# Kernel tuning notes

Hardware: AMD Instinct MI355X
Metric: run time of the kernel (lower is better)

The kernel has to match this reference:

```python
import jax, jax.numpy as jnp
import numpy as np

PHI = (1.0 + 5.0 ** 0.5) / 2.0
B, S, V, D, N, L = 8, 128, 32000, 256, 256, 2


def silu(x):
    return x * jax.nn.sigmoid(x)


def setup_inputs() -> dict:
    key = jax.random.key(0)
    ks = jax.random.split(key, 9)
    inp = {}
    inp["input_ids"] = jax.random.randint(ks[0], (B, S), 0, V)
    # token embedding, init std=0.02 as in _init_weights
    inp["emb"] = 0.02 * jax.random.normal(ks[1], (V, 2 * D), jnp.float32)
    # per-layer resonant params, stacked over layer dim L
    inp["ip_w"] = 0.02 * jax.random.normal(ks[2], (L, D, 2 * D), jnp.float32)  # input_proj weight
    inp["ip_b"] = jnp.zeros((L, D), jnp.float32)                                # input_proj bias
    inp["Wn"] = 0.02 * jax.random.normal(ks[3], (L, N, D), jnp.float32)         # W parameter
    inp["Bn"] = jnp.zeros((L, N, D), jnp.float32)                               # B parameter
    inp["opr"] = 0.02 * jax.random.normal(ks[4], (L, D, N), jnp.float32)        # out_proj_real
    inp["opi"] = 0.02 * jax.random.normal(ks[5], (L, D, N), jnp.float32)        # out_proj_imag
    inp["out_w"] = 0.02 * jax.random.normal(ks[6], (V, 2 * D), jnp.float32)     # output_proj
    inp["out_b"] = jnp.zeros((V,), jnp.float32)
    return inp


def _forward(input_ids, emb, ip_w, ip_b, Wn, Bn, opr, opi, out_w, out_b):
    tok = emb[input_ids]                                  # [B, S, 2D]
    w_emb = jnp.transpose(tok[..., :D], (1, 0, 2))        # [S, B, D] (time-major for scan)
    b_emb = jnp.transpose(tok[..., D:], (1, 0, 2))        # [S, B, D]
    ts = jnp.arange(S, dtype=jnp.float32)                 # t values

    def step(carry, xs):
        h_r, h_i = carry
        w_t, b_t, t = xs
        t_phi = t * PHI
        # Euler transform of recurrent state
        wl = 1.0 + jnp.abs(w_t)                           # [B, D]
        th_r = h_r / wl + b_t + t_phi
        th_i = h_i / wl + b_t + t_phi
        sr, cr = jnp.sin(th_r), jnp.cos(th_r)
        si, ci = jnp.sin(th_i), jnp.cos(th_i)
        h_r_new = cr * ci - sr * si                       # complex rotate
        h_i_new = cr * si + sr * ci
        x_r, x_i = h_r_new, h_i_new
        # resonant layers (residual deltas)
        for l in range(L):
            xc = jnp.concatenate([x_r, x_i], axis=-1) @ ip_w[l].T + ip_b[l]   # [B, D]
            wl_n = 1.0 + jnp.abs(Wn[l])                                        # [N, D]
            theta = xc[:, None, :] / wl_n + Bn[l] + t_phi                      # [B, N, D]
            cos_sum = jnp.cos(theta).sum(-1)                                   # [B, N]
            sin_sum = jnp.sin(theta).sum(-1)                                   # [B, N]
            x_r = x_r + silu(cos_sum @ opr[l].T)
            x_i = x_i + silu(sin_sum @ opi[l].T)
        logits = jnp.concatenate([x_r, x_i], axis=-1) @ out_w.T + out_b       # [B, V]
        return (h_r_new, h_i_new), logits

    h0 = jnp.zeros((B, D), jnp.float32)
    (_, _), logits = jax.lax.scan(step, (h0, h0), (w_emb, b_emb, ts))
    return jnp.transpose(logits, (1, 0, 2))               # [B, S, V]


def reference(input_ids, emb, ip_w, ip_b, Wn, Bn, opr, opi, out_w, out_b):
    return _forward(input_ids, emb, ip_w, ip_b, Wn, Bn, opr, opi, out_w, out_b)
```

## Files before the change

### kernel.cpp

```cpp
#include <hip/hip_runtime.h>
#include <hip/hip_fp16.h>
#include <math.h>


#define PHIF 1.6180339887498949f

typedef unsigned short u16;
typedef __attribute__((ext_vector_type(8))) _Float16 f16x8;
typedef __attribute__((ext_vector_type(4))) float f32x4;

constexpr int B = 8, S = 128, V = 32000, D = 256, N = 256, L = 2;
constexpr int TWO_D = 512;
constexpr int M = S * B;

constexpr size_t OFF_XR   = 0;
constexpr size_t OFF_XI   = OFF_XR   + (size_t)M * D;
constexpr size_t OFF_XC   = OFF_XI   + (size_t)M * D;
constexpr size_t OFF_CS   = OFF_XC   + (size_t)M * D;
constexpr size_t OFF_SS   = OFF_CS   + (size_t)M * N;
constexpr size_t OFF_RWT  = OFF_SS   + (size_t)M * N;
constexpr size_t OFF_BNT  = OFF_RWT  + (size_t)L * N * D;
constexpr size_t OFF_IPWT = OFF_BNT  + (size_t)L * N * D;
constexpr size_t OFF_OPRT = OFF_IPWT + (size_t)L * TWO_D * D;
constexpr size_t OFF_OPIT = OFF_OPRT + (size_t)L * N * D;
constexpr size_t OFF_FLT_END = OFF_OPIT + (size_t)L * N * D;

constexpr size_t A2_BYTE_OFF = OFF_FLT_END * 4;
constexpr size_t W2_BYTE_OFF = A2_BYTE_OFF + (size_t)M * 512 * 2;
constexpr size_t WS_NEED     = W2_BYTE_OFF + (size_t)V * 512 * 2;

__device__ __forceinline__ u16 f2h(float x) {
    return __half_as_ushort(__float2half(x));
}

__global__ void prep_kernel(const float* __restrict__ Wn,
                            const float* __restrict__ Bn,
                            const float* __restrict__ ip_w,
                            const float* __restrict__ opr,
                            const float* __restrict__ opi,
                            float* __restrict__ ws) {
    int i = blockIdx.x * blockDim.x + threadIdx.x;
    if (i < L * N * D) {
        int l = i >> 16;
        int r = i & 65535;
        int a = r >> 8;
        int c = r & 255;
        float wv = Wn[(size_t)l * N * D + (size_t)c * D + a];
        ws[OFF_RWT + i] = 1.0f / (1.0f + fabsf(wv));
        ws[OFF_BNT + i] = Bn[(size_t)l * N * D + (size_t)c * D + a];
        ws[OFF_OPRT + i] = opr[(size_t)l * D * N + (size_t)c * N + a];
        ws[OFF_OPIT + i] = opi[(size_t)l * D * N + (size_t)c * N + a];
    }
    if (i < L * TWO_D * D) {
        int l = i >> 17;
        int r = i & 131071;
        int k = r >> 8;
        int d = r & 255;
        ws[OFF_IPWT + i] = ip_w[(size_t)l * D * TWO_D + (size_t)d * TWO_D + k];
    }
}

__global__ __launch_bounds__(256) void conv_w_kernel(const float* __restrict__ out_w,
                                                     u16* __restrict__ W2) {
    int gid = blockIdx.x * blockDim.x + threadIdx.x;
    if (gid >= V * 128) return;
    int v  = gid >> 7;
    int kq = (gid & 127) << 2;
    float4 x = *(const float4*)&out_w[(size_t)v * TWO_D + kq];
    ushort4 h = {f2h(x.x), f2h(x.y), f2h(x.z), f2h(x.w)};
    *(ushort4*)&W2[(size_t)v * 512 + kq] = h;
}

__global__ __launch_bounds__(256) void conv_a_kernel(const float* __restrict__ ws,
                                                     u16* __restrict__ A2) {
    int gid = blockIdx.x * blockDim.x + threadIdx.x;
    if (gid >= M * 128) return;
    int m  = gid >> 7;
    int kq = (gid & 127) << 2;
    const float* XR = ws + OFF_XR;
    const float* XI = ws + OFF_XI;
    float4 x = (kq < D) ? *(const float4*)&XR[(size_t)m * D + kq]
                        : *(const float4*)&XI[(size_t)m * D + kq - D];
    ushort4 h = {f2h(x.x), f2h(x.y), f2h(x.z), f2h(x.w)};
    *(ushort4*)&A2[(size_t)m * 512 + kq] = h;
}

__global__ void recur_kernel(const int* __restrict__ ids,
                             const float* __restrict__ emb,
                             float* __restrict__ ws) {
    int tid = blockIdx.x * blockDim.x + threadIdx.x;
    if (tid >= B * D) return;
    int b = tid >> 8;
    int d = tid & 255;
    float* XR = ws + OFF_XR;
    float* XI = ws + OFF_XI;
    float hr = 0.f, hi = 0.f;
    for (int t = 0; t < S; ++t) {
        int id = ids[b * S + t];
        const float* e = emb + (size_t)id * TWO_D;
        float w  = e[d];
        float bb = e[D + d];
        float wl = 1.0f + fabsf(w);
        float tphi = (float)t * PHIF;
        float thr = hr / wl + bb + tphi;
        float thi = hi / wl + bb + tphi;
        float sr, cr, si, ci;
        sincosf(thr, &sr, &cr);
        sincosf(thi, &si, &ci);
        float nhr = cr * ci - sr * si;
        float nhi = cr * si + sr * ci;
        int row = t * B + b;
        XR[row * D + d] = nhr;
        XI[row * D + d] = nhi;
        hr = nhr; hi = nhi;
    }
}

__global__ __launch_bounds__(256) void xc_kernel(const float* __restrict__ ipb,
                                                 int l,
                                                 float* __restrict__ ws) {
    __shared__ float xrow[8][TWO_D];
    const float* XR = ws + OFF_XR;
    const float* XI = ws + OFF_XI;
    const float* WT = ws + OFF_IPWT + (size_t)l * TWO_D * D;
    float* XC = ws + OFF_XC;
    int m0 = blockIdx.x * 8;
    int tid = threadIdx.x;
    for (int j = 0; j < 16; ++j) {
        int idx = tid + j * 256;
        int r = idx >> 9;
        int k = idx & 511;
        xrow[r][k] = (k < D) ? XR[(m0 + r) * D + k] : XI[(m0 + r) * D + (k - D)];
    }
    __syncthreads();
    int d = tid;
    float bias = ipb[l * D + d];
    float acc[8];
    #pragma unroll
    for (int r = 0; r < 8; ++r) acc[r] = bias;
    for (int k = 0; k < TWO_D; ++k) {
        float wv = WT[k * D + d];
        #pragma unroll
        for (int r = 0; r < 8; ++r) acc[r] = fmaf(xrow[r][k], wv, acc[r]);
    }
    #pragma unroll
    for (int r = 0; r < 8; ++r) XC[(m0 + r) * D + d] = acc[r];
}

__global__ __launch_bounds__(256) void theta_kernel(int l, float* __restrict__ ws) {
    __shared__ float xls[2][D];
    const float* RWT = ws + OFF_RWT + (size_t)l * D * N;
    const float* BNT = ws + OFF_BNT + (size_t)l * D * N;
    const float* XC = ws + OFF_XC;
    float* CS = ws + OFF_CS;
    float* SS = ws + OFF_SS;
    int tb0 = blockIdx.x * 2;
    int n = threadIdx.x;
    xls[0][n] = XC[(size_t)tb0 * D + n];
    xls[1][n] = XC[(size_t)(tb0 + 1) * D + n];
    __syncthreads();
    float tp0 = (float)(tb0 >> 3) * PHIF;
    float tp1 = (float)((tb0 + 1) >> 3) * PHIF;
    float ac0 = 0.f, as0 = 0.f, ac1 = 0.f, as1 = 0.f;
    #pragma unroll 4
    for (int d = 0; d < D; ++d) {
        float rw = RWT[d * N + n];
        float bn = BNT[d * N + n];
        float th0 = fmaf(xls[0][d], rw, bn) + tp0;
        float th1 = fmaf(xls[1][d], rw, bn) + tp1;
        ac0 += __cosf(th0); as0 += __sinf(th0);
        ac1 += __cosf(th1); as1 += __sinf(th1);
    }
    CS[(size_t)tb0 * N + n] = ac0;
    SS[(size_t)tb0 * N + n] = as0;
    CS[(size_t)(tb0 + 1) * N + n] = ac1;
    SS[(size_t)(tb0 + 1) * N + n] = as1;
}

__global__ __launch_bounds__(256) void update_kernel(int l, float* __restrict__ ws) {
    __shared__ float csh[8][N];
    __shared__ float ssh[8][N];
    const float* CS = ws + OFF_CS;
    const float* SS = ws + OFF_SS;
    const float* WR = ws + OFF_OPRT + (size_t)l * N * D;
    const float* WI = ws + OFF_OPIT + (size_t)l * N * D;
    float* XR = ws + OFF_XR;
    float* XI = ws + OFF_XI;
    int m0 = blockIdx.x * 8;
    int tid = threadIdx.x;
    for (int j = 0; j < 8; ++j) {
        int idx = tid + j * 256;
        int r = idx >> 8;
        int n = idx & 255;
        csh[r][n] = CS[(m0 + r) * N + n];
        ssh[r][n] = SS[(m0 + r) * N + n];
    }
    __syncthreads();
    int d = tid;
    float accr[8] = {0,0,0,0,0,0,0,0};
    float acci[8] = {0,0,0,0,0,0,0,0};
    for (int n = 0; n < N; ++n) {
        float wr = WR[n * D + d];
        float wi = WI[n * D + d];
        #pragma unroll
        for (int r = 0; r < 8; ++r) {
            accr[r] = fmaf(csh[r][n], wr, accr[r]);
            acci[r] = fmaf(ssh[r][n], wi, acci[r]);
        }
    }
    #pragma unroll
    for (int r = 0; r < 8; ++r) {
        float vr = accr[r], vi = acci[r];
        float sgr = 1.0f / (1.0f + expf(-vr));
        float sgi = 1.0f / (1.0f + expf(-vi));
        XR[(m0 + r) * D + d] += vr * sgr;
        XI[(m0 + r) * D + d] += vi * sgi;
    }
}

__global__ __launch_bounds__(256) void logits_mfma_kernel(const u16* __restrict__ A2,
                                                          const u16* __restrict__ W2,
                                                          const float* __restrict__ out_b,
                                                          float* __restrict__ out) {
    __shared__ u16 sA[128 * 32];
    __shared__ u16 sW[128 * 32];
    int cb = blockIdx.x % (V / 128);
    int rb = blockIdx.x / (V / 128);
    int tid = threadIdx.x;
    int w = tid >> 6, l = tid & 63;
    int wr = w >> 1, wc = w & 1;

    f32x4 acc[4][4];
    #pragma unroll
    for (int i = 0; i < 4; ++i)
        #pragma unroll
        for (int j = 0; j < 4; ++j) acc[i][j] = (f32x4){0.f, 0.f, 0.f, 0.f};

    int srow = l >> 2;
    int sko  = (l & 3) * 8;
    int kg = (l >> 4) * 8;
    int rl = l & 15;

    for (int kk = 0; kk < 512; kk += 32) {
        #pragma unroll
        for (int j = 0; j < 2; ++j) {
            int rloc = (w * 2 + j) * 16 + srow;
            const u16* sa = A2 + (size_t)(rb * 128 + rloc) * 512 + kk + sko;
            const u16* sw = W2 + (size_t)(cb * 128 + rloc) * 512 + kk + sko;
            u16* da = &sA[rloc * 32 + sko];
            u16* dw = &sW[rloc * 32 + sko];
            __builtin_amdgcn_global_load_lds((const __attribute__((address_space(1))) void*)sa,
                                             (__attribute__((address_space(3))) void*)da, 16, 0, 0);
            __builtin_amdgcn_global_load_lds((const __attribute__((address_space(1))) void*)sw,
                                             (__attribute__((address_space(3))) void*)dw, 16, 0, 0);
        }
        __syncthreads();
        f16x8 af[4], wf[4];
        #pragma unroll
        for (int f = 0; f < 4; ++f) {
            af[f] = *(const f16x8*)&sA[(wr * 64 + f * 16 + rl) * 32 + kg];
            wf[f] = *(const f16x8*)&sW[(wc * 64 + f * 16 + rl) * 32 + kg];
        }
        #pragma unroll
        for (int fr = 0; fr < 4; ++fr)
            #pragma unroll
            for (int fc = 0; fc < 4; ++fc)
                acc[fr][fc] = __builtin_amdgcn_mfma_f32_16x16x32_f16(
                    af[fr], wf[fc], acc[fr][fc], 0, 0, 0);
        __syncthreads();
    }

    int rq = l >> 4;
    #pragma unroll
    for (int fc = 0; fc < 4; ++fc) {
        int v = cb * 128 + wc * 64 + fc * 16 + rl;
        float bv = out_b[v];
        #pragma unroll
        for (int fr = 0; fr < 4; ++fr) {
            #pragma unroll
            for (int r = 0; r < 4; ++r) {
                int row = rb * 128 + wr * 64 + fr * 16 + rq * 4 + r;
                int t = row >> 3, b = row & 7;
                out[((size_t)(b * S + t)) * V + v] = acc[fr][fc][r] + bv;
            }
        }
    }
}

constexpr int GBM = 256, GBN = 64, GBK = 32;
constexpr int LDA = GBM + 4;
constexpr int LDW = GBN + 4;

__global__ __launch_bounds__(256) void logits_kernel(const float* __restrict__ out_w,
                                                     const float* __restrict__ out_b,
                                                     const float* __restrict__ ws,
                                                     float* __restrict__ out) {
    __shared__ float As[GBK][LDA];
    __shared__ float Wsh[GBK][LDW];
    const float* XR = ws + OFF_XR;
    const float* XI = ws + OFF_XI;
    int cb = blockIdx.x % (V / GBN);
    int rb = blockIdx.x / (V / GBN);
    int tid = threadIdx.x;
    int tx = tid & 7;
    int ty = tid >> 3;
    int m_base = ty * 8;
    int n0 = tx * 8;
    float acc[8][8];
    #pragma unroll
    for (int r = 0; r < 8; ++r)
        #pragma unroll
        for (int c = 0; c < 8; ++c) acc[r][c] = 0.f;

    for (int kc = 0; kc < TWO_D; kc += GBK) {
        #pragma unroll
        for (int j = 0; j < 32; ++j) {
            int idx = tid + j * 256;
            int k = idx & 31;
            int m = idx >> 5;
            int kgl = kc + k;
            int row = rb * GBM + m;
            As[k][m] = (kgl < D) ? XR[row * D + kgl] : XI[row * D + (kgl - D)];
        }
        #pragma unroll
        for (int j = 0; j < 8; ++j) {
            int idx = tid + j * 256;
            int k = idx & 31;
            int n = idx >> 5;
            Wsh[k][n] = out_w[(size_t)(cb * GBN + n) * TWO_D + kc + k];
        }
        __syncthreads();
        #pragma unroll 8
        for (int k = 0; k < GBK; ++k) {
            float4 a0 = *(const float4*)&As[k][m_base];
            float4 a1 = *(const float4*)&As[k][m_base + 4];
            float4 w0 = *(const float4*)&Wsh[k][n0];
            float4 w1 = *(const float4*)&Wsh[k][n0 + 4];
            float am[8] = {a0.x, a0.y, a0.z, a0.w, a1.x, a1.y, a1.z, a1.w};
            float wn[8] = {w0.x, w0.y, w0.z, w0.w, w1.x, w1.y, w1.z, w1.w};
            #pragma unroll
            for (int r = 0; r < 8; ++r)
                #pragma unroll
                for (int c = 0; c < 8; ++c)
                    acc[r][c] = fmaf(am[r], wn[c], acc[r][c]);
        }
        __syncthreads();
    }
    int v0 = cb * GBN + n0;
    float4 ob0 = *(const float4*)&out_b[v0];
    float4 ob1 = *(const float4*)&out_b[v0 + 4];
    float obn[8] = {ob0.x, ob0.y, ob0.z, ob0.w, ob1.x, ob1.y, ob1.z, ob1.w};
    #pragma unroll
    for (int r = 0; r < 8; ++r) {
        int row = rb * GBM + m_base + r;
        int t = row >> 3;
        int b = row & 7;
        float o[8];
        #pragma unroll
        for (int c = 0; c < 8; ++c) o[c] = acc[r][c] + obn[c];
        *(float4*)&out[((size_t)(b * S + t)) * V + v0]     = *(float4*)&o[0];
        *(float4*)&out[((size_t)(b * S + t)) * V + v0 + 4] = *(float4*)&o[4];
    }
}

extern "C" void kernel_launch(void* const* d_in, const int* in_sizes, int n_in,
                              void* d_out, int out_size, void* d_ws, size_t ws_size,
                              hipStream_t stream) {
    const int*   ids   = (const int*)d_in[0];
    const float* emb   = (const float*)d_in[1];
    const float* ip_w  = (const float*)d_in[2];
    const float* ip_b  = (const float*)d_in[3];
    const float* Wn    = (const float*)d_in[4];
    const float* Bn    = (const float*)d_in[5];
    const float* opr   = (const float*)d_in[6];
    const float* opi   = (const float*)d_in[7];
    const float* out_w = (const float*)d_in[8];
    const float* out_b = (const float*)d_in[9];
    float* out = (float*)d_out;
    float* ws  = (float*)d_ws;
    const bool use_mfma = (ws_size >= WS_NEED);
    u16* A2 = (u16*)((char*)d_ws + A2_BYTE_OFF);
    u16* W2 = (u16*)((char*)d_ws + W2_BYTE_OFF);

    hipLaunchKernelGGL(prep_kernel,  dim3(1024), dim3(256), 0, stream, Wn, Bn, ip_w, opr, opi, ws);
    if (use_mfma)
        hipLaunchKernelGGL(conv_w_kernel, dim3(V * 128 / 256), dim3(256), 0, stream, out_w, W2);
    hipLaunchKernelGGL(recur_kernel, dim3(32),   dim3(64),  0, stream, ids, emb, ws);
    for (int l = 0; l < L; ++l) {
        hipLaunchKernelGGL(xc_kernel,     dim3(M / 8), dim3(256), 0, stream, ip_b, l, ws);
        hipLaunchKernelGGL(theta_kernel,  dim3(M / 2), dim3(256), 0, stream, l, ws);
        hipLaunchKernelGGL(update_kernel, dim3(M / 8), dim3(256), 0, stream, l, ws);
    }
    if (use_mfma) {
        hipLaunchKernelGGL(conv_a_kernel, dim3(M * 128 / 256), dim3(256), 0, stream, ws, A2);
        hipLaunchKernelGGL(logits_mfma_kernel, dim3((V / 128) * (M / 128)), dim3(256), 0, stream,
                           A2, W2, out_b, out);
    } else {
        hipLaunchKernelGGL(logits_kernel, dim3((V / GBN) * (M / GBM)), dim3(256), 0, stream,
                           out_w, out_b, ws, out);
    }
}
```

Baseline: 585.1 us.

## Collapse complex rotation into one phase and prefetch embeddings in recurrence

The recurrence is rewritten using the identity that the two rotations compose into a single angle, psi = (hr+hi)/wl + 2b + 2t*phi. Each step then needs one sin/cos pair, evaluated with the fast __sinf/__cosf intrinsics, instead of two full sincosf calls. Embedding rows for the whole sequence are prefetched into shared memory, which takes the dependent global loads off the serial critical path. Separately, the logits GEMM block order is swapped so consecutive blocks share a weight column tile, which should improve L2 reuse. The trade-off is that fast intrinsics on arguments reaching a few hundred radians may lose accuracy.

New measurement: 495.0 us. -15.4%, faster.

```diff
diff --git a/kernel.cpp b/kernel.cpp
--- a/kernel.cpp
+++ b/kernel.cpp
@@ -85,34 +85,40 @@
     *(ushort4*)&A2[(size_t)m * 512 + kq] = h;
 }
 
-__global__ void recur_kernel(const int* __restrict__ ids,
-                             const float* __restrict__ emb,
-                             float* __restrict__ ws) {
-    int tid = blockIdx.x * blockDim.x + threadIdx.x;
-    if (tid >= B * D) return;
-    int b = tid >> 8;
-    int d = tid & 255;
+__global__ __launch_bounds__(64) void recur_kernel(const int* __restrict__ ids,
+                                                   const float* __restrict__ emb,
+                                                   float* __restrict__ ws) {
+    __shared__ int   sid[S];
+    __shared__ float swv[S][64];
+    __shared__ float sbv[S][64];
+    int lane = threadIdx.x;
+    int blk  = blockIdx.x;
+    int b  = blk >> 2;
+    int d  = (blk & 3) * 64 + lane;
+    sid[lane]      = ids[b * S + lane];
+    sid[64 + lane] = ids[b * S + 64 + lane];
+    __syncthreads();
+    #pragma unroll 16
+    for (int t = 0; t < S; ++t) {
+        const float* e = emb + (size_t)sid[t] * TWO_D;
+        swv[t][lane] = e[d];
+        sbv[t][lane] = e[D + d];
+    }
+    __syncthreads();
     float* XR = ws + OFF_XR;
     float* XI = ws + OFF_XI;
-    float hr = 0.f, hi = 0.f;
+    float u = 0.f;
+    #pragma unroll 8
     for (int t = 0; t < S; ++t) {
-        int id = ids[b * S + t];
-        const float* e = emb + (size_t)id * TWO_D;
-        float w  = e[d];
-        float bb = e[D + d];
-        float wl = 1.0f + fabsf(w);
-        float tphi = (float)t * PHIF;
-        float thr = hr / wl + bb + tphi;
-        float thi = hi / wl + bb + tphi;
-        float sr, cr, si, ci;
-        sincosf(thr, &sr, &cr);
-        sincosf(thi, &si, &ci);
-        float nhr = cr * ci - sr * si;
-        float nhi = cr * si + sr * ci;
-        int row = t * B + b;
-        XR[row * D + d] = nhr;
-        XI[row * D + d] = nhi;
-        hr = nhr; hi = nhi;
+        float wl = 1.0f + fabsf(swv[t][lane]);
+        float c  = 2.0f * sbv[t][lane] + (2.0f * PHIF) * (float)t;
+        float psi = __fdividef(u, wl) + c;
+        float sn = __sinf(psi);
+        float cs = __cosf(psi);
+        size_t row = (size_t)(t * B + b) * D + d;
+        XR[row] = cs;
+        XI[row] = sn;
+        u = cs + sn;
     }
 }
 
@@ -224,8 +230,8 @@
                                                           float* __restrict__ out) {
     __shared__ u16 sA[128 * 32];
     __shared__ u16 sW[128 * 32];
-    int cb = blockIdx.x % (V / 128);
-    int rb = blockIdx.x / (V / 128);
+    int rb = blockIdx.x & 7;
+    int cb = blockIdx.x >> 3;
     int tid = threadIdx.x;
     int w = tid >> 6, l = tid & 63;
     int wr = w >> 1, wc = w & 1;
@@ -385,7 +391,7 @@
     hipLaunchKernelGGL(prep_kernel,  dim3(1024), dim3(256), 0, stream, Wn, Bn, ip_w, opr, opi, ws);
     if (use_mfma)
         hipLaunchKernelGGL(conv_w_kernel, dim3(V * 128 / 256), dim3(256), 0, stream, out_w, W2);
-    hipLaunchKernelGGL(recur_kernel, dim3(32),   dim3(64),  0, stream, ids, emb, ws);
+    hipLaunchKernelGGL(recur_kernel, dim3(32), dim3(64), 0, stream, ids, emb, ws);
     for (int l = 0; l < L; ++l) {
         hipLaunchKernelGGL(xc_kernel,     dim3(M / 8), dim3(256), 0, stream, ip_b, l, ws);
         hipLaunchKernelGGL(theta_kernel,  dim3(M / 2), dim3(256), 0, stream, l, ws);
```
